# Kernel optimization log

Hardware: AMD Instinct MI355X
Metric: run time of the kernel (lower is better)

## Reference

```python
import jax, jax.numpy as jnp
import numpy as np

N = 1_000_000
D_IN = 64
D_HID = 128
NUM_SEG = 8192


def setup_inputs() -> dict:
    key = jax.random.key(0)
    ks = jax.random.split(key, 8)
    f_all = jax.random.normal(ks[0], (N, D_IN), dtype=jnp.float32)
    seg_ids = jnp.sort(jax.random.randint(ks[1], (N,), 0, NUM_SEG, dtype=jnp.int32))
    W1 = jax.random.normal(ks[2], (D_IN, 32), dtype=jnp.float32) * 0.1
    b1 = jax.random.normal(ks[3], (32,), dtype=jnp.float32) * 0.1
    W2 = jax.random.normal(ks[4], (32, 64), dtype=jnp.float32) * 0.1
    b2 = jax.random.normal(ks[5], (64,), dtype=jnp.float32) * 0.1
    W3 = jax.random.normal(ks[6], (64, D_HID), dtype=jnp.float32) * 0.1
    b3 = jax.random.normal(ks[7], (D_HID,), dtype=jnp.float32) * 0.1
    return {"f_all": f_all, "seg_ids": seg_ids, "num_segments": NUM_SEG,
            "W1": W1, "b1": b1, "W2": W2, "b2": b2, "W3": W3, "b3": b3}


def reference(f_all, seg_ids, num_segments, W1, b1, W2, b2, W3, b3):
    # 3-layer MLP: input -> 32 -> 64 -> hidden_size, ReLU on first two
    y = jax.nn.relu(f_all @ W1 + b1)          # [N, 32]
    y = jax.nn.relu(y @ W2 + b2)              # [N, 64]
    y = y @ W3 + b3                           # [N, hidden]
    # per-segment mean; empty segments stay zero (matches torch.zeros init)
    sums = jax.ops.segment_sum(y, seg_ids, num_segments=num_segments)           # [S, hidden]
    counts = jax.ops.segment_sum(jnp.ones((f_all.shape[0],), y.dtype), seg_ids,
                                 num_segments=num_segments)                     # [S]
    return sums / jnp.maximum(counts, 1.0)[:, None]
```

## Files before the change

### kernel.cpp

```cpp
#include <hip/hip_runtime.h>

constexpr int D_IN  = 64;
constexpr int D_H1  = 32;
constexpr int D_H2  = 64;
constexpr int D_OUT = 128;
constexpr int NSEG  = 8192;

constexpr int BLOCK = 256;
constexpr int RT    = 64;
constexpr int TPB   = 8;
constexpr int SYS   = D_OUT + 8;

typedef __bf16 bfx8 __attribute__((ext_vector_type(8)));
typedef __bf16 bfx4 __attribute__((ext_vector_type(4)));
typedef float  fx4  __attribute__((ext_vector_type(4)));


__global__ __launch_bounds__(BLOCK, 3) void mlp_seg_mfma(
    const float* __restrict__ f, const int* __restrict__ seg,
    const float* __restrict__ W1, const float* __restrict__ b1,
    const float* __restrict__ W2, const float* __restrict__ b2,
    const float* __restrict__ W3, const float* __restrict__ b3,
    float* __restrict__ sums, float* __restrict__ counts,
    int N, int ntiles)
{
    __shared__ __align__(16) __bf16 sf [RT * 64];
    __shared__ __align__(16) __bf16 sh1[RT * 32];
    __shared__ __align__(16) __bf16 sh2[RT * 64];
    __shared__ __align__(16) __bf16 sy [RT * SYS];
    __shared__ int sseg[RT];

    const int tid  = threadIdx.x;
    const int wv   = tid >> 6;
    const int lane = tid & 63;
    const int lr   = lane & 15;
    const int quad = lane >> 4;
    const int m0   = wv * 16;
    const int ar   = m0 + lr;

    bfx8 fw1[2][2];
    #pragma unroll
    for (int j = 0; j < 2; ++j)
        #pragma unroll
        for (int ks = 0; ks < 2; ++ks)
            #pragma unroll
            for (int i = 0; i < 8; ++i)
                fw1[j][ks][i] = (__bf16)W1[(ks*32 + quad*8 + i)*D_H1 + j*16 + lr];

    bfx8 fw2[4];
    #pragma unroll
    for (int j = 0; j < 4; ++j)
        #pragma unroll
        for (int i = 0; i < 8; ++i)
            fw2[j][i] = (__bf16)W2[(quad*8 + i)*D_H2 + j*16 + lr];

    bfx8 fw3[8][2];
    #pragma unroll
    for (int j = 0; j < 8; ++j)
        #pragma unroll
        for (int ks = 0; ks < 2; ++ks)
            #pragma unroll
            for (int i = 0; i < 8; ++i)
                fw3[j][ks][i] = (__bf16)W3[(ks*32 + quad*8 + i)*D_OUT + j*16 + lr];

    float rb1[2], rb2[4], rb3[8];
    #pragma unroll
    for (int j = 0; j < 2; ++j) rb1[j] = b1[j*16 + lr];
    #pragma unroll
    for (int j = 0; j < 4; ++j) rb2[j] = b2[j*16 + lr];
    #pragma unroll
    for (int j = 0; j < 8; ++j) rb3[j] = b3[j*16 + lr];

    const int colA = tid & 127;
    const int grp  = tid >> 7;
    int   cur_seg = -1;
    float run_sum = 0.f;
    int   run_len = 0;

    const int t0 = blockIdx.x * TPB;
    const int t1 = min(t0 + TPB, ntiles);

    for (int t = t0; t < t1; ++t) {
        const int R0 = t * RT;

        const float4* f4 = (const float4*)f + (size_t)R0 * 16;
        #pragma unroll
        for (int i = 0; i < 4; ++i) {
            const int idx4 = tid + i * 256;
            float4 q = make_float4(0.f, 0.f, 0.f, 0.f);
            if ((size_t)R0 * 64 + (size_t)idx4 * 4 < (size_t)N * 64) q = f4[idx4];
            const int r = idx4 >> 4;
            const int c = (idx4 & 15) * 4;
            bfx4 v;
            v[0] = (__bf16)q.x; v[1] = (__bf16)q.y;
            v[2] = (__bf16)q.z; v[3] = (__bf16)q.w;
            const int pe = r*64 + ((((c >> 3) ^ (r & 7))) << 3) + (c & 7);
            *(bfx4*)&sf[pe] = v;
        }
        if (tid < RT) sseg[tid] = (R0 + tid < N) ? seg[R0 + tid] : -2;
        __syncthreads();

        fx4 acc1[2] = {{0,0,0,0},{0,0,0,0}};
        #pragma unroll
        for (int ks = 0; ks < 2; ++ks) {
            bfx8 a = *(const bfx8*)&sf[ar*64 + (((ks*4 + quad) ^ (ar & 7)) << 3)];
            #pragma unroll
            for (int j = 0; j < 2; ++j)
                acc1[j] = __builtin_amdgcn_mfma_f32_16x16x32_bf16(a, fw1[j][ks], acc1[j], 0, 0, 0);
        }
        #pragma unroll
        for (int j = 0; j < 2; ++j)
            #pragma unroll
            for (int rg = 0; rg < 4; ++rg) {
                const int row = m0 + quad*4 + rg;
                const int col = j*16 + lr;
                const float v = fmaxf(acc1[j][rg] + rb1[j], 0.f);
                sh1[row*32 + (((col >> 3) ^ (row & 3)) << 3) + (col & 7)] = (__bf16)v;
            }

        fx4 acc2[4] = {{0,0,0,0},{0,0,0,0},{0,0,0,0},{0,0,0,0}};
        {
            bfx8 a = *(const bfx8*)&sh1[ar*32 + ((quad ^ (ar & 3)) << 3)];
            #pragma unroll
            for (int j = 0; j < 4; ++j)
                acc2[j] = __builtin_amdgcn_mfma_f32_16x16x32_bf16(a, fw2[j], acc2[j], 0, 0, 0);
        }
        #pragma unroll
        for (int j = 0; j < 4; ++j)
            #pragma unroll
            for (int rg = 0; rg < 4; ++rg) {
                const int row = m0 + quad*4 + rg;
                const int col = j*16 + lr;
                const float v = fmaxf(acc2[j][rg] + rb2[j], 0.f);
                sh2[row*64 + (((col >> 3) ^ (row & 7)) << 3) + (col & 7)] = (__bf16)v;
            }

        #pragma unroll
        for (int h = 0; h < 2; ++h) {
            fx4 acc3[4] = {{0,0,0,0},{0,0,0,0},{0,0,0,0},{0,0,0,0}};
            #pragma unroll
            for (int ks = 0; ks < 2; ++ks) {
                bfx8 a = *(const bfx8*)&sh2[ar*64 + (((ks*4 + quad) ^ (ar & 7)) << 3)];
                #pragma unroll
                for (int j = 0; j < 4; ++j)
                    acc3[j] = __builtin_amdgcn_mfma_f32_16x16x32_bf16(a, fw3[h*4 + j][ks], acc3[j], 0, 0, 0);
            }
            #pragma unroll
            for (int j = 0; j < 4; ++j)
                #pragma unroll
                for (int rg = 0; rg < 4; ++rg) {
                    const int row = m0 + quad*4 + rg;
                    const int col = (h*4 + j)*16 + lr;
                    sy[row*SYS + col] = (__bf16)(acc3[j][rg] + rb3[h*4 + j]);
                }
        }
        __syncthreads();

        for (int rr = 0; rr < 32; ++rr) {
            const int r = grp*32 + rr;
            const int s = sseg[r];
            const float v = (float)sy[r*SYS + colA];
            if (s != cur_seg) {
                if (cur_seg >= 0) {
                    atomicAdd(&sums[(size_t)cur_seg * D_OUT + colA], run_sum);
                    if (colA == 0) atomicAdd(&counts[cur_seg], (float)run_len);
                }
                cur_seg = s; run_sum = 0.f; run_len = 0;
            }
            run_sum += v; run_len++;
        }
        __syncthreads();
    }

    if (cur_seg >= 0) {
        atomicAdd(&sums[(size_t)cur_seg * D_OUT + colA], run_sum);
        if (colA == 0) atomicAdd(&counts[cur_seg], (float)run_len);
    }
}

__global__ __launch_bounds__(256) void div_kernel(
    const float* __restrict__ sums, const float* __restrict__ counts,
    float* __restrict__ out, int total)
{
    const int i = blockIdx.x * 256 + threadIdx.x;
    if (i < total) out[i] = sums[i] / fmaxf(counts[i >> 7], 1.f);
}

extern "C" void kernel_launch(void* const* d_in, const int* in_sizes, int n_in,
                              void* d_out, int out_size, void* d_ws, size_t ws_size,
                              hipStream_t stream) {
    const float* f   = (const float*)d_in[0];
    const int*   seg = (const int*)  d_in[1];
    const float* W1 = (const float*)d_in[3];
    const float* b1 = (const float*)d_in[4];
    const float* W2 = (const float*)d_in[5];
    const float* b2 = (const float*)d_in[6];
    const float* W3 = (const float*)d_in[7];
    const float* b3 = (const float*)d_in[8];
    float* out = (float*)d_out;

    const int N = in_sizes[0] / D_IN;

    float* sums   = (float*)d_ws;
    float* counts = sums + (size_t)NSEG * D_OUT;

    hipMemsetAsync(d_ws, 0, ((size_t)NSEG * D_OUT + NSEG) * sizeof(float), stream);

    const int ntiles  = (N + RT - 1) / RT;
    const int nblocks = (ntiles + TPB - 1) / TPB;
    mlp_seg_mfma<<<nblocks, BLOCK, 0, stream>>>(f, seg, W1, b1, W2, b2, W3, b3,
                                                sums, counts, N, ntiles);

    const int total = NSEG * D_OUT;
    div_kernel<<<(total + 255) / 256, 256, 0, stream>>>(sums, counts, out, total);
}
```

Baseline: 477.8 us.

## Prefetch next tile into registers and reduce segments via ballot-based run detection

Loads the next tile's features and segment ids into registers while the current tile's MLP runs, so global memory latency overlaps compute. Replaces the per-row serial scan with a ballot over segment boundaries: each half-block sums its rows per run, partial sums are combined through shared memory, and only one half issues atomics. Also raises the occupancy hint from 3 to 4 blocks and narrows the output tile stride in LDS to 132. The trade-offs are more register pressure from the prefetch buffers and extra barriers whenever a tile holds more than four segments.

```diff
diff --git a/kernel.cpp b/kernel.cpp
--- a/kernel.cpp
+++ b/kernel.cpp
@@ -9,14 +9,14 @@
 constexpr int BLOCK = 256;
 constexpr int RT    = 64;
 constexpr int TPB   = 8;
-constexpr int SYS   = D_OUT + 8;
+constexpr int SYS   = 132;
 
 typedef __bf16 bfx8 __attribute__((ext_vector_type(8)));
 typedef __bf16 bfx4 __attribute__((ext_vector_type(4)));
 typedef float  fx4  __attribute__((ext_vector_type(4)));
 
 
-__global__ __launch_bounds__(BLOCK, 3) void mlp_seg_mfma(
+__global__ __launch_bounds__(BLOCK, 4) void mlp_seg_mfma(
     const float* __restrict__ f, const int* __restrict__ seg,
     const float* __restrict__ W1, const float* __restrict__ b1,
     const float* __restrict__ W2, const float* __restrict__ b2,
@@ -28,6 +28,7 @@
     __shared__ __align__(16) __bf16 sh1[RT * 32];
     __shared__ __align__(16) __bf16 sh2[RT * 64];
     __shared__ __align__(16) __bf16 sy [RT * SYS];
+    __shared__ float pbuf[4 * 128];
     __shared__ int sseg[RT];
 
     const int tid  = threadIdx.x;
@@ -71,34 +72,55 @@
     #pragma unroll
     for (int j = 0; j < 8; ++j) rb3[j] = b3[j*16 + lr];
 
-    const int colA = tid & 127;
-    const int grp  = tid >> 7;
+    const int col = tid & 127;
+    const int hh  = tid >> 7;
     int   cur_seg = -1;
     float run_sum = 0.f;
-    int   run_len = 0;
+    int   run_cnt = 0;
 
     const int t0 = blockIdx.x * TPB;
     const int t1 = min(t0 + TPB, ntiles);
 
-    for (int t = t0; t < t1; ++t) {
-        const int R0 = t * RT;
-
-        const float4* f4 = (const float4*)f + (size_t)R0 * 16;
+    float4 q[4];
+    int segv = -2;
+    {
+        const size_t base4 = (size_t)t0 * RT * 16;
+        const float4* f4 = (const float4*)f;
         #pragma unroll
         for (int i = 0; i < 4; ++i) {
             const int idx4 = tid + i * 256;
-            float4 q = make_float4(0.f, 0.f, 0.f, 0.f);
-            if ((size_t)R0 * 64 + (size_t)idx4 * 4 < (size_t)N * 64) q = f4[idx4];
+            q[i] = make_float4(0.f, 0.f, 0.f, 0.f);
+            if ((base4 + idx4) * 4 < (size_t)N * 64) q[i] = f4[base4 + idx4];
+        }
+        if (tid < RT) segv = (t0 * RT + tid < N) ? seg[t0 * RT + tid] : -2;
+    }
+
+    for (int t = t0; t < t1; ++t) {
+        #pragma unroll
+        for (int i = 0; i < 4; ++i) {
+            const int idx4 = tid + i * 256;
             const int r = idx4 >> 4;
             const int c = (idx4 & 15) * 4;
             bfx4 v;
-            v[0] = (__bf16)q.x; v[1] = (__bf16)q.y;
-            v[2] = (__bf16)q.z; v[3] = (__bf16)q.w;
+            v[0] = (__bf16)q[i].x; v[1] = (__bf16)q[i].y;
+            v[2] = (__bf16)q[i].z; v[3] = (__bf16)q[i].w;
             const int pe = r*64 + ((((c >> 3) ^ (r & 7))) << 3) + (c & 7);
             *(bfx4*)&sf[pe] = v;
         }
-        if (tid < RT) sseg[tid] = (R0 + tid < N) ? seg[R0 + tid] : -2;
+        if (tid < RT) sseg[tid] = segv;
         __syncthreads();
+
+        if (t + 1 < t1) {
+            const size_t base4 = (size_t)(t + 1) * RT * 16;
+            const float4* f4 = (const float4*)f;
+            #pragma unroll
+            for (int i = 0; i < 4; ++i) {
+                const int idx4 = tid + i * 256;
+                q[i] = make_float4(0.f, 0.f, 0.f, 0.f);
+                if ((base4 + idx4) * 4 < (size_t)N * 64) q[i] = f4[base4 + idx4];
+            }
+            if (tid < RT) segv = ((t+1) * RT + tid < N) ? seg[(t+1) * RT + tid] : -2;
+        }
 
         fx4 acc1[2] = {{0,0,0,0},{0,0,0,0}};
         #pragma unroll
@@ -113,9 +135,9 @@
             #pragma unroll
             for (int rg = 0; rg < 4; ++rg) {
                 const int row = m0 + quad*4 + rg;
-                const int col = j*16 + lr;
+                const int cc  = j*16 + lr;
                 const float v = fmaxf(acc1[j][rg] + rb1[j], 0.f);
-                sh1[row*32 + (((col >> 3) ^ (row & 3)) << 3) + (col & 7)] = (__bf16)v;
+                sh1[row*32 + (((cc >> 3) ^ (row & 3)) << 3) + (cc & 7)] = (__bf16)v;
             }
 
         fx4 acc2[4] = {{0,0,0,0},{0,0,0,0},{0,0,0,0},{0,0,0,0}};
@@ -130,9 +152,9 @@
             #pragma unroll
             for (int rg = 0; rg < 4; ++rg) {
                 const int row = m0 + quad*4 + rg;
-                const int col = j*16 + lr;
+                const int cc  = j*16 + lr;
                 const float v = fmaxf(acc2[j][rg] + rb2[j], 0.f);
-                sh2[row*64 + (((col >> 3) ^ (row & 7)) << 3) + (col & 7)] = (__bf16)v;
+                sh2[row*64 + (((cc >> 3) ^ (row & 7)) << 3) + (cc & 7)] = (__bf16)v;
             }
 
         #pragma unroll
@@ -150,31 +172,63 @@
                 #pragma unroll
                 for (int rg = 0; rg < 4; ++rg) {
                     const int row = m0 + quad*4 + rg;
-                    const int col = (h*4 + j)*16 + lr;
-                    sy[row*SYS + col] = (__bf16)(acc3[j][rg] + rb3[h*4 + j]);
+                    const int cc  = (h*4 + j)*16 + lr;
+                    sy[row*SYS + cc] = (__bf16)(acc3[j][rg] + rb3[h*4 + j]);
                 }
         }
         __syncthreads();
 
-        for (int rr = 0; rr < 32; ++rr) {
-            const int r = grp*32 + rr;
-            const int s = sseg[r];
-            const float v = (float)sy[r*SYS + colA];
-            if (s != cur_seg) {
-                if (cur_seg >= 0) {
-                    atomicAdd(&sums[(size_t)cur_seg * D_OUT + colA], run_sum);
-                    if (colA == 0) atomicAdd(&counts[cur_seg], (float)run_len);
+        const int prev = (lane == 0) ? -999999 : sseg[lane - 1];
+        const unsigned long long bmask = __ballot(sseg[lane] != prev);
+        const int nuniq = __popcll(bmask);
+
+        unsigned long long mrem = bmask;
+        for (int base = 0; base < nuniq; base += 4) {
+            const int nk = min(4, nuniq - base);
+            float pk[4]; int sk[4]; int ck[4];
+            unsigned long long mit = mrem;
+            for (int k = 0; k < nk; ++k) {
+                const int st = __ffsll((long long)mit) - 1;
+                const unsigned long long mnx = mit & (mit - 1);
+                const int en = mnx ? (__ffsll((long long)mnx) - 1) : RT;
+                sk[k] = sseg[st];
+                ck[k] = en - st;
+                const int lo = max(st, hh * 32);
+                const int hi = min(en, hh * 32 + 32);
+                float a0 = 0.f, a1 = 0.f;
+                for (int r = lo; r < hi; r += 2) {
+                    a0 += (float)sy[r * SYS + col];
+                    if (r + 1 < hi) a1 += (float)sy[(r + 1) * SYS + col];
                 }
-                cur_seg = s; run_sum = 0.f; run_len = 0;
-            }
-            run_sum += v; run_len++;
-        }
-        __syncthreads();
+                pk[k] = a0 + a1;
+                mit = mnx;
+            }
+            mrem = mit;
+            if (hh == 1) {
+                for (int k = 0; k < nk; ++k) pbuf[k * 128 + col] = pk[k];
+            }
+            __syncthreads();
+            if (hh == 0) {
+                for (int k = 0; k < nk; ++k) {
+                    const int s = sk[k];
+                    const float val = pk[k] + pbuf[k * 128 + col];
+                    if (s != cur_seg) {
+                        if (cur_seg >= 0) {
+                            atomicAdd(&sums[(size_t)cur_seg * D_OUT + col], run_sum);
+                            if (col == 0) atomicAdd(&counts[cur_seg], (float)run_cnt);
+                        }
+                        cur_seg = s; run_sum = 0.f; run_cnt = 0;
+                    }
+                    run_sum += val; run_cnt += ck[k];
+                }
+            }
+            if (base + 4 < nuniq) __syncthreads();
+        }
     }
 
-    if (cur_seg >= 0) {
-        atomicAdd(&sums[(size_t)cur_seg * D_OUT + colA], run_sum);
-        if (colA == 0) atomicAdd(&counts[cur_seg], (float)run_len);
+    if (hh == 0 && cur_seg >= 0) {
+        atomicAdd(&sums[(size_t)cur_seg * D_OUT + col], run_sum);
+        if (col == 0) atomicAdd(&counts[cur_seg], (float)run_cnt);
     }
 }
 
```

After: 704.6 us. +47.5%, slower.
